# Kernel tuning notes

Hardware: AMD Instinct MI355X
Metric: run time of the kernel (lower is better)

Reference implementation:

```python
import math
import jax, jax.numpy as jnp
import numpy as np

FACTOR = 1  # init factor; top_k = max(1, int(FACTOR * log(L)))


def setup_inputs() -> dict:
    key = jax.random.key(0)
    kq, kk, kv = jax.random.split(key, 3)
    B, L, H, E = 8, 4096, 8, 64
    queries = jax.random.normal(kq, (B, L, H, E), dtype=jnp.float32)
    keys = jax.random.normal(kk, (B, L, H, E), dtype=jnp.float32)
    values = jax.random.normal(kv, (B, L, H, E), dtype=jnp.float32)
    return {"queries": queries, "keys": keys, "values": values}


def reference(queries, keys, values):
    # queries/keys: [B, L, H, E], values: [B, L, H, D] (L == S so no padding branch)
    B, L, H, E = queries.shape
    q = jnp.transpose(queries, (0, 2, 3, 1))  # [B, H, E, L]
    k = jnp.transpose(keys, (0, 2, 3, 1))
    v = jnp.transpose(values, (0, 2, 3, 1))   # [B, H, D, L]

    # FFT-based circular cross-correlation along time axis
    qf = jnp.fft.rfft(q, axis=-1)
    kf = jnp.fft.rfft(k, axis=-1)
    corr = jnp.fft.irfft(qf * jnp.conj(kf), n=L, axis=-1)  # [B, H, E, L]

    # Inference-time delay aggregation (eval path of the module)
    top_k = max(1, int(FACTOR * math.log(L)))
    mean_corr = corr.mean(axis=(1, 2))                      # [B, L]
    w_top, idx_top = jax.lax.top_k(mean_corr, top_k)        # [B, K]
    w = jax.nn.softmax(w_top, axis=-1)                      # [B, K]

    # circular shift: out[..., t] = sum_i w_i * v[..., (t + delay_i) mod L]
    t = jnp.arange(L)
    idx = (t[None, None, :] + idx_top[:, :, None]) % L      # [B, K, L]
    gathered = jnp.take_along_axis(
        v[:, None], idx[:, :, None, None, :], axis=-1
    )                                                       # [B, K, H, D, L]
    agg = jnp.einsum('bkhdl,bk->bhdl', gathered, w)         # [B, H, D, L]
    return jnp.transpose(agg, (0, 3, 1, 2))                 # [B, L, H, D]
```

## Files before the change

### kernel.cpp

```cpp
#include <hip/hip_runtime.h>
#include <math.h>


namespace {
constexpr int LEN  = 4096;
constexpr int NCH  = 512;
constexpr int NB   = 8;
constexpr int KTOP = 8;
constexpr int TPB  = 256;
constexpr int CPB  = 4;
constexpr int GPB  = NCH / CPB;
constexpr size_t SF_BYTES = (size_t)NB * LEN * 2 * sizeof(float);
constexpr size_t WI_BYTES = (size_t)NB * KTOP * sizeof(float);
constexpr size_t ZT_OFF   = SF_BYTES + 2 * WI_BYTES;
constexpr size_t ZT_BYTES = (size_t)NB * NCH * LEN * 2 * sizeof(float);
constexpr int PADN = LEN + (LEN >> 4);
}

#define PD(i) ((i) + ((i) >> 4))

__device__ __forceinline__ float2 cmul(float2 a, float2 b) {
  return make_float2(a.x * b.x - a.y * b.y, a.x * b.y + a.y * b.x);
}

__device__ __forceinline__ void dft16(const float2* __restrict__ a,
                                      float2* __restrict__ b) {
  const float C1 = 0.92387953251128674f;
  const float S1 = 0.38268343236508978f;
  const float R2 = 0.70710678118654752f;
  float2 c[4][4];
  #pragma unroll
  for (int r0 = 0; r0 < 4; ++r0) {
    const float2 x0 = a[r0], x1 = a[4 + r0], x2 = a[8 + r0], x3 = a[12 + r0];
    const float2 s02 = make_float2(x0.x + x2.x, x0.y + x2.y);
    const float2 d02 = make_float2(x0.x - x2.x, x0.y - x2.y);
    const float2 s13 = make_float2(x1.x + x3.x, x1.y + x3.y);
    const float2 d13 = make_float2(x1.x - x3.x, x1.y - x3.y);
    c[r0][0] = make_float2(s02.x + s13.x, s02.y + s13.y);
    c[r0][2] = make_float2(s02.x - s13.x, s02.y - s13.y);
    c[r0][1] = make_float2(d02.x + d13.y, d02.y - d13.x);
    c[r0][3] = make_float2(d02.x - d13.y, d02.y + d13.x);
  }
  #pragma unroll
  for (int k0 = 0; k0 < 4; ++k0) {
    float2 t0 = c[0][k0], t1 = c[1][k0], t2 = c[2][k0], t3 = c[3][k0];
    if (k0 == 1) {
      t1 = cmul(t1, make_float2(C1, -S1));
      t2 = cmul(t2, make_float2(R2, -R2));
      t3 = cmul(t3, make_float2(S1, -C1));
    } else if (k0 == 2) {
      t1 = cmul(t1, make_float2(R2, -R2));
      t2 = make_float2(t2.y, -t2.x);
      t3 = cmul(t3, make_float2(-R2, -R2));
    } else if (k0 == 3) {
      t1 = cmul(t1, make_float2(S1, -C1));
      t2 = cmul(t2, make_float2(-R2, -R2));
      t3 = cmul(t3, make_float2(-C1, S1));
    }
    const float2 s02 = make_float2(t0.x + t2.x, t0.y + t2.y);
    const float2 d02 = make_float2(t0.x - t2.x, t0.y - t2.y);
    const float2 s13 = make_float2(t1.x + t3.x, t1.y + t3.y);
    const float2 d13 = make_float2(t1.x - t3.x, t1.y - t3.y);
    b[k0]      = make_float2(s02.x + s13.x, s02.y + s13.y);
    b[k0 + 8]  = make_float2(s02.x - s13.x, s02.y - s13.y);
    b[k0 + 4]  = make_float2(d02.x + d13.y, d02.y - d13.x);
    b[k0 + 12] = make_float2(d02.x - d13.y, d02.y + d13.x);
  }
}

__device__ __forceinline__ void fft4096_ip(float2* __restrict__ buf, int tid)
{
  float2 a[16], b[16];
  const float NEG2PI_N = -6.283185307179586f / 4096.0f;
  {
    #pragma unroll
    for (int r = 0; r < 16; ++r) a[r] = buf[PD(tid + 256 * r)];
    dft16(a, b);
    float sn, cs;
    __sincosf((float)tid * NEG2PI_N, &sn, &cs);
    const float2 w1 = make_float2(cs, sn);
    __syncthreads();
    float2 w = make_float2(1.f, 0.f);
    #pragma unroll
    for (int k = 0; k < 16; ++k) {
      buf[PD(16 * tid + k)] = cmul(b[k], w);
      w = cmul(w, w1);
    }
  }
  __syncthreads();
  {
    const int q = tid & 15, p = tid >> 4;
    #pragma unroll
    for (int r = 0; r < 16; ++r) a[r] = buf[PD(tid + 256 * r)];
    dft16(a, b);
    float sn, cs;
    __sincosf((float)(16 * p) * NEG2PI_N, &sn, &cs);
    const float2 w1 = make_float2(cs, sn);
    __syncthreads();
    float2 w = make_float2(1.f, 0.f);
    const int ob = q + 256 * p;
    #pragma unroll
    for (int k = 0; k < 16; ++k) {
      buf[PD(ob + 16 * k)] = cmul(b[k], w);
      w = cmul(w, w1);
    }
  }
  __syncthreads();
  {
    #pragma unroll
    for (int r = 0; r < 16; ++r) a[r] = buf[PD(tid + 256 * r)];
    dft16(a, b);
    __syncthreads();
    #pragma unroll
    for (int k = 0; k < 16; ++k) buf[PD(tid + 256 * k)] = b[k];
  }
  __syncthreads();
}

__global__ __launch_bounds__(TPB) void k_transpose(
    const float* __restrict__ qg, const float* __restrict__ kg,
    float2* __restrict__ zt)
{
  __shared__ float2 tile[64 * 65];
  const int bt  = blockIdx.x;
  const int b   = bt >> 9;
  const int t0  = ((bt >> 3) & 63) * 64;
  const int c0  = (bt & 7) * 64;
  const int tid = threadIdx.x;
  const size_t base = (size_t)b * LEN * NCH;

  #pragma unroll
  for (int r = 0; r < 16; ++r) {
    const int idx  = r * TPB + tid;
    const int ch_l = idx & 63;
    const int t_l  = idx >> 6;
    const size_t g = base + (size_t)(t0 + t_l) * NCH + (c0 + ch_l);
    tile[t_l * 65 + ch_l] = make_float2(qg[g], kg[g]);
  }
  __syncthreads();
  #pragma unroll
  for (int r = 0; r < 16; ++r) {
    const int idx  = r * TPB + tid;
    const int t_l  = idx & 63;
    const int ch_l = idx >> 6;
    zt[((size_t)b * NCH + (c0 + ch_l)) * LEN + (t0 + t_l)] =
        tile[t_l * 65 + ch_l];
  }
}

__device__ __forceinline__ void spec_acc(const float2* __restrict__ buf,
                                         int tid, float2* __restrict__ acc)
{
  #pragma unroll
  for (int r = 0; r < 16; ++r) {
    const int f = tid + 256 * r;
    const float2 A = buf[PD(f)];
    float2 Bv = buf[PD((LEN - f) & (LEN - 1))];
    Bv.y = -Bv.y;
    const float Sx = A.x + Bv.x, Sy = A.y + Bv.y;
    const float Dx = A.x - Bv.x, Dy = -(A.y - Bv.y);
    const float Mx = Sx * Dx - Sy * Dy;
    const float My = Sx * Dy + Sy * Dx;
    acc[r].x += -0.25f * My;
    acc[r].y +=  0.25f * Mx;
  }
}

__global__ __launch_bounds__(TPB) void k_fft_corr(
    const float2* __restrict__ zt,
    float* __restrict__ Sf)
{
  __shared__ float2 buf[PADN];
  const int tid = threadIdx.x;
  const int b   = blockIdx.x / GPB;
  const int g   = blockIdx.x % GPB;
  const int ch0 = g * CPB;

  float2 acc[16];
  #pragma unroll
  for (int r = 0; r < 16; ++r) acc[r] = make_float2(0.f, 0.f);

  for (int cc = 0; cc < CPB; ++cc) {
    const float4* src =
        (const float4*)(zt + ((size_t)b * NCH + (ch0 + cc)) * LEN);
    #pragma unroll
    for (int r = 0; r < 8; ++r) {
      const float4 x = src[tid + 256 * r];
      const int t = 2 * (tid + 256 * r);
      buf[PD(t)]     = make_float2(x.x, x.y);
      buf[PD(t + 1)] = make_float2(x.z, x.w);
    }
    __syncthreads();
    fft4096_ip(buf, tid);
    spec_acc(buf, tid, acc);
    __syncthreads();
  }
  float* dstp = Sf + (size_t)b * LEN * 2;
  #pragma unroll
  for (int r = 0; r < 16; ++r) {
    const int f = tid + 256 * r;
    atomicAdd(&dstp[2 * f],     acc[r].x);
    atomicAdd(&dstp[2 * f + 1], acc[r].y);
  }
}

__global__ __launch_bounds__(TPB) void k_fft_corr_strided(
    const float* __restrict__ qg, const float* __restrict__ kg,
    float* __restrict__ Sf)
{
  __shared__ float2 buf[PADN];
  const int tid = threadIdx.x;
  const int b   = blockIdx.x / GPB;
  const int g   = blockIdx.x % GPB;
  const int ch0 = g * CPB;

  float2 acc[16];
  #pragma unroll
  for (int r = 0; r < 16; ++r) acc[r] = make_float2(0.f, 0.f);

  const size_t base = (size_t)b * LEN * NCH;
  for (int cc = 0; cc < CPB; ++cc) {
    const int ch = ch0 + cc;
    #pragma unroll
    for (int r = 0; r < 16; ++r) {
      const int t = tid + 256 * r;
      const size_t idx = base + (size_t)t * NCH + ch;
      buf[PD(t)] = make_float2(qg[idx], kg[idx]);
    }
    __syncthreads();
    fft4096_ip(buf, tid);
    spec_acc(buf, tid, acc);
    __syncthreads();
  }
  float* dstp = Sf + (size_t)b * LEN * 2;
  #pragma unroll
  for (int r = 0; r < 16; ++r) {
    const int f = tid + 256 * r;
    atomicAdd(&dstp[2 * f],     acc[r].x);
    atomicAdd(&dstp[2 * f + 1], acc[r].y);
  }
}

__global__ __launch_bounds__(TPB) void k_ifft_topk(
    const float* __restrict__ Sf,
    float* __restrict__ wout, int* __restrict__ iout)
{
  __shared__ float2 buf[PADN];
  __shared__ float swv[4];
  __shared__ int   swi[4];
  __shared__ int   gsel;
  __shared__ float topv[KTOP];
  __shared__ int   topi[KTOP];
  const int tid = threadIdx.x;
  const int b   = blockIdx.x;

  const float2* srcp = (const float2*)Sf + (size_t)b * LEN;
  #pragma unroll
  for (int r = 0; r < 16; ++r) {
    const int f = tid + 256 * r;
    const float2 s = srcp[f];
    buf[PD(f)] = make_float2(s.x, -s.y);
  }
  __syncthreads();
  fft4096_ip(buf, tid);

  const float scale = 1.0f / (4096.0f * 512.0f);
  float rv[16];
  #pragma unroll
  for (int r = 0; r < 16; ++r) rv[r] = buf[PD(tid + 256 * r)].x * scale;

  const int lane = tid & 63, wv = tid >> 6;
  for (int it = 0; it < KTOP; ++it) {
    float best = -INFINITY;
    int   bi   = 0x7fffffff;
    #pragma unroll
    for (int r = 0; r < 16; ++r) {
      if (rv[r] > best) { best = rv[r]; bi = tid + 256 * r; }
    }
    #pragma unroll
    for (int off = 32; off > 0; off >>= 1) {
      const float ov = __shfl_xor(best, off);
      const int   oi = __shfl_xor(bi, off);
      if (ov > best || (ov == best && oi < bi)) { best = ov; bi = oi; }
    }
    if (lane == 0) { swv[wv] = best; swi[wv] = bi; }
    __syncthreads();
    if (tid == 0) {
      float gv = swv[0]; int gi = swi[0];
      for (int w2 = 1; w2 < 4; ++w2)
        if (swv[w2] > gv || (swv[w2] == gv && swi[w2] < gi)) {
          gv = swv[w2]; gi = swi[w2];
        }
      topv[it] = gv; topi[it] = gi; gsel = gi;
    }
    __syncthreads();
    const int gi = gsel;
    if ((gi & 255) == tid) {
      const int rr = gi >> 8;
      #pragma unroll
      for (int r = 0; r < 16; ++r)
        if (r == rr) rv[r] = -INFINITY;
    }
  }
  if (tid == 0) {
    const float m = topv[0];
    float e[KTOP], den = 0.f;
    #pragma unroll
    for (int i = 0; i < KTOP; ++i) { e[i] = expf(topv[i] - m); den += e[i]; }
    #pragma unroll
    for (int i = 0; i < KTOP; ++i) {
      wout[b * KTOP + i] = e[i] / den;
      iout[b * KTOP + i] = topi[i];
    }
  }
}

__global__ __launch_bounds__(256) void k_gather(
    const float4* __restrict__ v, const float* __restrict__ wk,
    const int* __restrict__ ik, float4* __restrict__ out)
{
  __shared__ float sw[KTOP];
  __shared__ int   sidx[KTOP];
  const int b  = blockIdx.x >> 11;
  const int tp = blockIdx.x & 2047;
  if (threadIdx.x < KTOP) {
    sw[threadIdx.x]   = wk[b * KTOP + threadIdx.x];
    sidx[threadIdx.x] = ik[b * KTOP + threadIdx.x];
  }
  __syncthreads();
  const int t = tp * 2 + (threadIdx.x >> 7);
  const int c = threadIdx.x & 127;
  const size_t vbase = (size_t)b * LEN * 128;
  float4 acc = make_float4(0.f, 0.f, 0.f, 0.f);
  #pragma unroll
  for (int i = 0; i < KTOP; ++i) {
    const int st = (t + sidx[i]) & (LEN - 1);
    const float4 x = v[vbase + (size_t)st * 128 + c];
    acc.x += sw[i] * x.x; acc.y += sw[i] * x.y;
    acc.z += sw[i] * x.z; acc.w += sw[i] * x.w;
  }
  out[vbase + (size_t)t * 128 + c] = acc;
}

extern "C" void kernel_launch(void* const* d_in, const int* in_sizes, int n_in,
                              void* d_out, int out_size, void* d_ws, size_t ws_size,
                              hipStream_t stream) {
  const float* q = (const float*)d_in[0];
  const float* k = (const float*)d_in[1];
  const float* v = (const float*)d_in[2];

  float*  Sf = (float*)d_ws;
  float*  wk = (float*)((char*)d_ws + SF_BYTES);
  int*    ik = (int*)((char*)d_ws + SF_BYTES + WI_BYTES);
  float2* zt = (float2*)((char*)d_ws + ZT_OFF);

  hipMemsetAsync(d_ws, 0, SF_BYTES, stream);
  if (ws_size >= ZT_OFF + ZT_BYTES) {
    k_transpose<<<NB * 64 * 8, TPB, 0, stream>>>(q, k, zt);
    k_fft_corr<<<NB * GPB, TPB, 0, stream>>>(zt, Sf);
  } else {
    k_fft_corr_strided<<<NB * GPB, TPB, 0, stream>>>(q, k, Sf);
  }
  k_ifft_topk<<<NB, TPB, 0, stream>>>(Sf, wk, ik);
  k_gather<<<NB * 2048, 256, 0, stream>>>((const float4*)v, wk, ik,
                                          (float4*)(float*)d_out);
}
```

Measured before the change: 403.4 us.

## Prefetch next channel into LDS via async global loads while computing FFT

The correlation FFT kernel now double-buffers its input. It uses global_load_lds to stream the next channel's data into a separate LDS staging buffer while the current channel's three-pass radix-16 FFT runs, with hand-placed waitcnt barriers. The FFT is inlined with twiddles generated on the fly by sincos recurrence, and each block now handles 8 channels instead of 4, which halves the atomic accumulations. This aims to hide global-memory latency, at the cost of extra LDS use (lower occupancy) and some twiddle precision drift from the recurrence.

```diff
diff --git a/kernel.cpp b/kernel.cpp
--- a/kernel.cpp
+++ b/kernel.cpp
@@ -8,7 +8,7 @@
 constexpr int NB   = 8;
 constexpr int KTOP = 8;
 constexpr int TPB  = 256;
-constexpr int CPB  = 4;
+constexpr int CPB  = 8;
 constexpr int GPB  = NCH / CPB;
 constexpr size_t SF_BYTES = (size_t)NB * LEN * 2 * sizeof(float);
 constexpr size_t WI_BYTES = (size_t)NB * KTOP * sizeof(float);
@@ -22,6 +22,23 @@
 __device__ __forceinline__ float2 cmul(float2 a, float2 b) {
   return make_float2(a.x * b.x - a.y * b.y, a.x * b.y + a.y * b.x);
 }
+
+__device__ __forceinline__ void gload_lds16(const void* g, void* l) {
+  __builtin_amdgcn_global_load_lds(
+      (const __attribute__((address_space(1))) void*)g,
+      (__attribute__((address_space(3))) void*)l, 16, 0, 0);
+}
+
+#define LGKM_BAR()                                          \
+  do {                                                      \
+    asm volatile("s_waitcnt lgkmcnt(0)" ::: "memory");      \
+    __builtin_amdgcn_s_barrier();                           \
+  } while (0)
+#define FULL_BAR()                                          \
+  do {                                                      \
+    asm volatile("s_waitcnt vmcnt(0) lgkmcnt(0)" ::: "memory"); \
+    __builtin_amdgcn_s_barrier();                           \
+  } while (0)
 
 __device__ __forceinline__ void dft16(const float2* __restrict__ a,
                                       float2* __restrict__ b) {
@@ -170,30 +187,81 @@
     const float2* __restrict__ zt,
     float* __restrict__ Sf)
 {
-  __shared__ float2 buf[PADN];
-  const int tid = threadIdx.x;
-  const int b   = blockIdx.x / GPB;
-  const int g   = blockIdx.x % GPB;
-  const int ch0 = g * CPB;
+  __shared__ float2 bufA[PADN];
+  __shared__ float2 bufS[LEN];
+  const int tid  = threadIdx.x;
+  const int lane = tid & 63;
+  const int wv   = tid >> 6;
+  const int b    = blockIdx.x / GPB;
+  const int g    = blockIdx.x % GPB;
+  const float2* base = zt + ((size_t)b * NCH + g * CPB) * LEN;
 
   float2 acc[16];
   #pragma unroll
   for (int r = 0; r < 16; ++r) acc[r] = make_float2(0.f, 0.f);
 
+  {
+    const char* gs = (const char*)base + (size_t)wv * 8192 + (size_t)lane * 16;
+    char* ls = (char*)bufS + wv * 8192;
+    #pragma unroll
+    for (int i = 0; i < 8; ++i)
+      gload_lds16(gs + i * 1024, ls + i * 1024);
+  }
+  FULL_BAR();
+
+  const float NEG2PI_N = -6.283185307179586f / 4096.0f;
   for (int cc = 0; cc < CPB; ++cc) {
-    const float4* src =
-        (const float4*)(zt + ((size_t)b * NCH + (ch0 + cc)) * LEN);
-    #pragma unroll
-    for (int r = 0; r < 8; ++r) {
-      const float4 x = src[tid + 256 * r];
-      const int t = 2 * (tid + 256 * r);
-      buf[PD(t)]     = make_float2(x.x, x.y);
-      buf[PD(t + 1)] = make_float2(x.z, x.w);
-    }
-    __syncthreads();
-    fft4096_ip(buf, tid);
-    spec_acc(buf, tid, acc);
-    __syncthreads();
+    float2 a[16], bb[16];
+    float sn, cs;
+    #pragma unroll
+    for (int r = 0; r < 16; ++r) a[r] = bufS[tid + 256 * r];
+    LGKM_BAR();
+    if (cc + 1 < CPB) {
+      const char* gs = (const char*)(base + (size_t)(cc + 1) * LEN)
+                       + (size_t)wv * 8192 + (size_t)lane * 16;
+      char* ls = (char*)bufS + wv * 8192;
+      #pragma unroll
+      for (int i = 0; i < 8; ++i)
+        gload_lds16(gs + i * 1024, ls + i * 1024);
+    }
+    dft16(a, bb);
+    __sincosf((float)tid * NEG2PI_N, &sn, &cs);
+    {
+      const float2 w1 = make_float2(cs, sn);
+      float2 w = make_float2(1.f, 0.f);
+      #pragma unroll
+      for (int k = 0; k < 16; ++k) {
+        bufA[PD(16 * tid + k)] = cmul(bb[k], w);
+        w = cmul(w, w1);
+      }
+    }
+    LGKM_BAR();
+    #pragma unroll
+    for (int r = 0; r < 16; ++r) a[r] = bufA[PD(tid + 256 * r)];
+    LGKM_BAR();
+    dft16(a, bb);
+    {
+      const int qq = tid & 15, p = tid >> 4;
+      __sincosf((float)(16 * p) * NEG2PI_N, &sn, &cs);
+      const float2 w1 = make_float2(cs, sn);
+      float2 w = make_float2(1.f, 0.f);
+      const int ob = qq + 256 * p;
+      #pragma unroll
+      for (int k = 0; k < 16; ++k) {
+        bufA[PD(ob + 16 * k)] = cmul(bb[k], w);
+        w = cmul(w, w1);
+      }
+    }
+    LGKM_BAR();
+    #pragma unroll
+    for (int r = 0; r < 16; ++r) a[r] = bufA[PD(tid + 256 * r)];
+    LGKM_BAR();
+    dft16(a, bb);
+    #pragma unroll
+    for (int k = 0; k < 16; ++k) bufA[PD(tid + 256 * k)] = bb[k];
+    LGKM_BAR();
+    spec_acc(bufA, tid, acc);
+    FULL_BAR();
   }
   float* dstp = Sf + (size_t)b * LEN * 2;
   #pragma unroll
@@ -363,5 +431,5 @@
   }
   k_ifft_topk<<<NB, TPB, 0, stream>>>(Sf, wk, ik);
   k_gather<<<NB * 2048, 256, 0, stream>>>((const float4*)v, wk, ik,
-                                          (float4*)(float*)d_out);
-}
+                                          (float4*)d_out);
+}
```

Result: faster. 362.1 us (-10.2%).
